# Performance work log

Measured on AMD Instinct MI355X. Metric: run time of the kernel, lower is better.

Reference implementation:

```python
import jax, jax.numpy as jnp
import numpy as np

L, D = 8192, 2048


def setup_inputs() -> dict:
    key = jax.random.key(0)
    kx, kA, kB, kC = jax.random.split(key, 4)
    x = jax.random.normal(kx, (L, D), dtype=jnp.float32)
    A = jax.random.normal(kA, (D,), dtype=jnp.float32)
    B = jax.random.normal(kB, (D,), dtype=jnp.float32)
    C = jax.random.normal(kC, (D,), dtype=jnp.float32)
    return {"x": x, "A": A, "B": B, "C": C}


def reference(x, A, B, C):
    # state_t = A * state_{t-1} + B * x_t ; y_t = tanh(C * state_t)
    Bx = B * x  # [L, D], precompute input injection

    def step(state, bx_t):
        state = A * state + bx_t
        return state, jnp.tanh(C * state)

    _, ys = jax.lax.scan(step, jnp.zeros((D,), dtype=x.dtype), Bx)
    return ys  # [L, D]
```

## Files before the change

### kernel.cpp

```cpp
#include <hip/hip_runtime.h>
#include <math.h>


#define LL 8192
#define DD 2048
#define CL 32
#define NC (LL / CL)
#define G4 (DD / 4)

__global__ __launch_bounds__(256) void mamba_p1(
    const float4* __restrict__ x4, const float4* __restrict__ A4,
    const float4* __restrict__ B4, float4* __restrict__ loc4)
{
    int lin   = blockIdx.x * 256 + threadIdx.x;
    int chunk = lin >> 9;
    int grp   = lin & (G4 - 1);

    float4 a = A4[grp];
    float4 b = B4[grp];
    float sx = 0.f, sy = 0.f, sz = 0.f, sw = 0.f;

    const float4* xp = x4 + (size_t)chunk * CL * G4 + grp;
    #pragma unroll
    for (int t = 0; t < CL; ++t) {
        float4 v = xp[(size_t)t * G4];
        sx = fmaf(a.x, sx, b.x * v.x);
        sy = fmaf(a.y, sy, b.y * v.y);
        sz = fmaf(a.z, sz, b.z * v.z);
        sw = fmaf(a.w, sw, b.w * v.w);
    }
    loc4[(size_t)chunk * G4 + grp] = make_float4(sx, sy, sz, sw);
}

__global__ __launch_bounds__(64) void mamba_p2(
    const float* __restrict__ A, const float* __restrict__ loc,
    float* __restrict__ car)
{
    int ch = blockIdx.x * 64 + threadIdx.x;
    float a = A[ch];

    float p = a;
    #pragma unroll
    for (int i = 0; i < 5; ++i) p *= p;

    float c = 0.f;
    for (int c0 = 0; c0 < NC; c0 += 64) {
        float lv[64];
        #pragma unroll
        for (int k = 0; k < 64; ++k)
            lv[k] = loc[(size_t)(c0 + k) * DD + ch];
        #pragma unroll
        for (int k = 0; k < 64; ++k) {
            car[(size_t)(c0 + k) * DD + ch] = c;
            c = fmaf(p, c, lv[k]);
        }
    }
}

__device__ __forceinline__ float fast_tanh(float z)
{
    float e = __builtin_amdgcn_exp2f(z * 2.885390081777927f);
    return 1.0f - 2.0f * __builtin_amdgcn_rcpf(e + 1.0f);
}

__global__ __launch_bounds__(256) void mamba_p3(
    const float4* __restrict__ x4, const float4* __restrict__ A4,
    const float4* __restrict__ B4, const float4* __restrict__ C4,
    const float4* __restrict__ car4, float4* __restrict__ y4)
{
    int lin   = blockIdx.x * 256 + threadIdx.x;
    int chunk = lin >> 9;
    int grp   = lin & (G4 - 1);

    float4 a = A4[grp];
    float4 b = B4[grp];
    float4 c = C4[grp];
    float4 s0 = car4[(size_t)chunk * G4 + grp];
    float sx = s0.x, sy = s0.y, sz = s0.z, sw = s0.w;

    const float4* xp = x4 + (size_t)chunk * CL * G4 + grp;
    float4*       yp = y4 + (size_t)chunk * CL * G4 + grp;

    #pragma unroll 8
    for (int t = 0; t < CL; ++t) {
        float4 v = xp[(size_t)t * G4];
        sx = fmaf(a.x, sx, b.x * v.x);
        sy = fmaf(a.y, sy, b.y * v.y);
        sz = fmaf(a.z, sz, b.z * v.z);
        sw = fmaf(a.w, sw, b.w * v.w);
        float4 o = make_float4(fast_tanh(c.x * sx), fast_tanh(c.y * sy),
                               fast_tanh(c.z * sz), fast_tanh(c.w * sw));
        yp[(size_t)t * G4] = o;
    }
}

extern "C" void kernel_launch(void* const* d_in, const int* in_sizes, int n_in,
                              void* d_out, int out_size, void* d_ws, size_t ws_size,
                              hipStream_t stream)
{
    const float*  Af = (const float*)d_in[1];
    const float4* x4 = (const float4*)d_in[0];
    const float4* A4 = (const float4*)d_in[1];
    const float4* B4 = (const float4*)d_in[2];
    const float4* C4 = (const float4*)d_in[3];
    float4* y4 = (float4*)d_out;

    float*  locf = (float*)d_ws;
    float4* loc4 = (float4*)d_ws;
    float*  carf = locf + (size_t)NC * DD;
    float4* car4 = (float4*)carf;

    const int nthreads = NC * G4;
    mamba_p1<<<nthreads / 256, 256, 0, stream>>>(x4, A4, B4, loc4);
    mamba_p2<<<DD / 64, 64, 0, stream>>>(Af, locf, carf);
    mamba_p3<<<nthreads / 256, 256, 0, stream>>>(x4, A4, B4, C4, car4, y4);
}
```

Baseline: 48.39 us.

## Fuse three scan passes into one persistent kernel with atomic grid barriers

Replaces the three launches (per-chunk local scan, cross-chunk carry scan, final recompute with tanh) with one kernel. The 32 x rows each thread needs stay in registers across phases, so x is read once instead of twice. Global atomic counters act as grid-wide barriers: 8 blocks run the carry scan while the other blocks spin on a counter. Output uses nontemporal stores. The design relies on all 512 blocks being co-resident (launch bounds of 2 blocks per CU), so it risks deadlock or a serial stall if occupancy is lower. It also adds a memset and high register pressure.

```diff
diff --git a/kernel.cpp b/kernel.cpp
--- a/kernel.cpp
+++ b/kernel.cpp
@@ -7,48 +7,144 @@
 #define CL 32
 #define NC (LL / CL)
 #define G4 (DD / 4)
+#define NBLK (NC * G4 / 256)
+#define NSCAN (DD / 256)
+
+typedef float f32x4 __attribute__((ext_vector_type(4)));
+
+__device__ __forceinline__ float fast_tanh(float z)
+{
+    float e = __builtin_amdgcn_exp2f(z * 2.885390081777927f);
+    return 1.0f - 2.0f * __builtin_amdgcn_rcpf(e + 1.0f);
+}
+
+__global__ __launch_bounds__(256, 2) void mamba_fused(
+    const float4* __restrict__ x4, const float4* __restrict__ A4,
+    const float4* __restrict__ B4, const float4* __restrict__ C4,
+    float4* __restrict__ loc4, float4* __restrict__ car4,
+    unsigned* __restrict__ cnt, float4* __restrict__ y4)
+{
+    const int lin   = blockIdx.x * 256 + threadIdx.x;
+    const int chunk = lin >> 9;
+    const int grp   = lin & (G4 - 1);
+
+    const float4 a = A4[grp];
+    const float4 b = B4[grp];
+
+    const size_t base = (size_t)chunk * CL * G4 + grp;
+
+    float4 xr[CL];
+    #pragma unroll
+    for (int t = 0; t < CL; ++t) xr[t] = x4[base + (size_t)t * G4];
+
+    float sx = 0.f, sy = 0.f, sz = 0.f, sw = 0.f;
+    #pragma unroll
+    for (int t = 0; t < CL; ++t) {
+        sx = fmaf(a.x, sx, b.x * xr[t].x);
+        sy = fmaf(a.y, sy, b.y * xr[t].y);
+        sz = fmaf(a.z, sz, b.z * xr[t].z);
+        sw = fmaf(a.w, sw, b.w * xr[t].w);
+    }
+    loc4[(size_t)chunk * G4 + grp] = make_float4(sx, sy, sz, sw);
+
+    __syncthreads();
+    if (threadIdx.x == 0) {
+        __threadfence();
+        __hip_atomic_fetch_add(&cnt[0], 1u, __ATOMIC_RELAXED, __HIP_MEMORY_SCOPE_AGENT);
+    }
+
+    if (blockIdx.x < NSCAN) {
+        if (threadIdx.x == 0) {
+            while (__hip_atomic_load(&cnt[0], __ATOMIC_RELAXED, __HIP_MEMORY_SCOPE_AGENT) < NBLK)
+                __builtin_amdgcn_s_sleep(2);
+            __threadfence();
+        }
+        __syncthreads();
+
+        const int ch = blockIdx.x * 256 + threadIdx.x;
+        const float* loc = (const float*)loc4;
+        float*       car = (float*)car4;
+
+        float p = ((const float*)A4)[ch];
+        #pragma unroll
+        for (int i = 0; i < 5; ++i) p *= p;
+
+        float c = 0.f;
+        for (int c0 = 0; c0 < NC; c0 += 32) {
+            float lv[32];
+            #pragma unroll
+            for (int k = 0; k < 32; ++k)
+                lv[k] = loc[(size_t)(c0 + k) * DD + ch];
+            #pragma unroll
+            for (int k = 0; k < 32; ++k) {
+                car[(size_t)(c0 + k) * DD + ch] = c;
+                c = fmaf(p, c, lv[k]);
+            }
+        }
+
+        __syncthreads();
+        if (threadIdx.x == 0) {
+            __threadfence();
+            __hip_atomic_fetch_add(&cnt[1], 1u, __ATOMIC_RELAXED, __HIP_MEMORY_SCOPE_AGENT);
+        }
+    }
+
+    if (threadIdx.x == 0) {
+        while (__hip_atomic_load(&cnt[1], __ATOMIC_RELAXED, __HIP_MEMORY_SCOPE_AGENT) < NSCAN)
+            __builtin_amdgcn_s_sleep(2);
+        __threadfence();
+    }
+    __syncthreads();
+
+    const float4 cc = C4[grp];
+    float4 s0 = car4[(size_t)chunk * G4 + grp];
+    sx = s0.x; sy = s0.y; sz = s0.z; sw = s0.w;
+
+    #pragma unroll
+    for (int t = 0; t < CL; ++t) {
+        sx = fmaf(a.x, sx, b.x * xr[t].x);
+        sy = fmaf(a.y, sy, b.y * xr[t].y);
+        sz = fmaf(a.z, sz, b.z * xr[t].z);
+        sw = fmaf(a.w, sw, b.w * xr[t].w);
+        f32x4 o;
+        o.x = fast_tanh(cc.x * sx);
+        o.y = fast_tanh(cc.y * sy);
+        o.z = fast_tanh(cc.z * sz);
+        o.w = fast_tanh(cc.w * sw);
+        __builtin_nontemporal_store(o, (f32x4*)&y4[base + (size_t)t * G4]);
+    }
+}
 
 __global__ __launch_bounds__(256) void mamba_p1(
     const float4* __restrict__ x4, const float4* __restrict__ A4,
     const float4* __restrict__ B4, float4* __restrict__ loc4)
 {
-    int lin   = blockIdx.x * 256 + threadIdx.x;
-    int chunk = lin >> 9;
-    int grp   = lin & (G4 - 1);
-
-    float4 a = A4[grp];
-    float4 b = B4[grp];
+    int lin = blockIdx.x * 256 + threadIdx.x;
+    int chunk = lin >> 9, grp = lin & (G4 - 1);
+    float4 a = A4[grp], b = B4[grp];
     float sx = 0.f, sy = 0.f, sz = 0.f, sw = 0.f;
-
     const float4* xp = x4 + (size_t)chunk * CL * G4 + grp;
     #pragma unroll
     for (int t = 0; t < CL; ++t) {
         float4 v = xp[(size_t)t * G4];
-        sx = fmaf(a.x, sx, b.x * v.x);
-        sy = fmaf(a.y, sy, b.y * v.y);
-        sz = fmaf(a.z, sz, b.z * v.z);
-        sw = fmaf(a.w, sw, b.w * v.w);
+        sx = fmaf(a.x, sx, b.x * v.x); sy = fmaf(a.y, sy, b.y * v.y);
+        sz = fmaf(a.z, sz, b.z * v.z); sw = fmaf(a.w, sw, b.w * v.w);
     }
     loc4[(size_t)chunk * G4 + grp] = make_float4(sx, sy, sz, sw);
 }
 
 __global__ __launch_bounds__(64) void mamba_p2(
-    const float* __restrict__ A, const float* __restrict__ loc,
-    float* __restrict__ car)
+    const float* __restrict__ A, const float* __restrict__ loc, float* __restrict__ car)
 {
     int ch = blockIdx.x * 64 + threadIdx.x;
-    float a = A[ch];
-
-    float p = a;
+    float p = A[ch];
     #pragma unroll
     for (int i = 0; i < 5; ++i) p *= p;
-
     float c = 0.f;
     for (int c0 = 0; c0 < NC; c0 += 64) {
         float lv[64];
         #pragma unroll
-        for (int k = 0; k < 64; ++k)
-            lv[k] = loc[(size_t)(c0 + k) * DD + ch];
+        for (int k = 0; k < 64; ++k) lv[k] = loc[(size_t)(c0 + k) * DD + ch];
         #pragma unroll
         for (int k = 0; k < 64; ++k) {
             car[(size_t)(c0 + k) * DD + ch] = c;
@@ -57,40 +153,25 @@
     }
 }
 
-__device__ __forceinline__ float fast_tanh(float z)
-{
-    float e = __builtin_amdgcn_exp2f(z * 2.885390081777927f);
-    return 1.0f - 2.0f * __builtin_amdgcn_rcpf(e + 1.0f);
-}
-
 __global__ __launch_bounds__(256) void mamba_p3(
     const float4* __restrict__ x4, const float4* __restrict__ A4,
     const float4* __restrict__ B4, const float4* __restrict__ C4,
     const float4* __restrict__ car4, float4* __restrict__ y4)
 {
-    int lin   = blockIdx.x * 256 + threadIdx.x;
-    int chunk = lin >> 9;
-    int grp   = lin & (G4 - 1);
-
-    float4 a = A4[grp];
-    float4 b = B4[grp];
-    float4 c = C4[grp];
+    int lin = blockIdx.x * 256 + threadIdx.x;
+    int chunk = lin >> 9, grp = lin & (G4 - 1);
+    float4 a = A4[grp], b = B4[grp], c = C4[grp];
     float4 s0 = car4[(size_t)chunk * G4 + grp];
     float sx = s0.x, sy = s0.y, sz = s0.z, sw = s0.w;
-
     const float4* xp = x4 + (size_t)chunk * CL * G4 + grp;
     float4*       yp = y4 + (size_t)chunk * CL * G4 + grp;
-
     #pragma unroll 8
     for (int t = 0; t < CL; ++t) {
         float4 v = xp[(size_t)t * G4];
-        sx = fmaf(a.x, sx, b.x * v.x);
-        sy = fmaf(a.y, sy, b.y * v.y);
-        sz = fmaf(a.z, sz, b.z * v.z);
-        sw = fmaf(a.w, sw, b.w * v.w);
-        float4 o = make_float4(fast_tanh(c.x * sx), fast_tanh(c.y * sy),
-                               fast_tanh(c.z * sz), fast_tanh(c.w * sw));
-        yp[(size_t)t * G4] = o;
+        sx = fmaf(a.x, sx, b.x * v.x); sy = fmaf(a.y, sy, b.y * v.y);
+        sz = fmaf(a.z, sz, b.z * v.z); sw = fmaf(a.w, sw, b.w * v.w);
+        yp[(size_t)t * G4] = make_float4(fast_tanh(c.x * sx), fast_tanh(c.y * sy),
+                                         fast_tanh(c.z * sz), fast_tanh(c.w * sw));
     }
 }
 
@@ -98,20 +179,27 @@
                               void* d_out, int out_size, void* d_ws, size_t ws_size,
                               hipStream_t stream)
 {
-    const float*  Af = (const float*)d_in[1];
     const float4* x4 = (const float4*)d_in[0];
     const float4* A4 = (const float4*)d_in[1];
     const float4* B4 = (const float4*)d_in[2];
     const float4* C4 = (const float4*)d_in[3];
     float4* y4 = (float4*)d_out;
 
-    float*  locf = (float*)d_ws;
     float4* loc4 = (float4*)d_ws;
-    float*  carf = locf + (size_t)NC * DD;
-    float4* car4 = (float4*)carf;
-
-    const int nthreads = NC * G4;
-    mamba_p1<<<nthreads / 256, 256, 0, stream>>>(x4, A4, B4, loc4);
-    mamba_p2<<<DD / 64, 64, 0, stream>>>(Af, locf, carf);
-    mamba_p3<<<nthreads / 256, 256, 0, stream>>>(x4, A4, B4, C4, car4, y4);
-}
+    float4* car4 = loc4 + (size_t)NC * G4;
+    const size_t body = (size_t)NC * DD * 4 * 2;
+
+    if (ws_size >= body + 16) {
+        unsigned* cnt = (unsigned*)((char*)d_ws + body);
+        (void)hipMemsetAsync(cnt, 0, 16, stream);
+        mamba_fused<<<NBLK, 256, 0, stream>>>(x4, A4, B4, C4, loc4, car4, cnt, y4);
+    } else {
+        const float* Af  = (const float*)d_in[1];
+        float* locf = (float*)loc4;
+        float* carf = (float*)car4;
+        const int nthreads = NC * G4;
+        mamba_p1<<<nthreads / 256, 256, 0, stream>>>(x4, A4, B4, loc4);
+        mamba_p2<<<DD / 64, 64, 0, stream>>>(Af, locf, carf);
+        mamba_p3<<<nthreads / 256, 256, 0, stream>>>(x4, A4, B4, C4, car4, y4);
+    }
+}
```

Measured after the change: 101.5 us. +109.7%, slower.
